# Kernel optimization log

Hardware: AMD Instinct MI355X
Metric: run time of the kernel (lower is better)

## Reference

```python
import jax, jax.numpy as jnp
import numpy as np

B, C, L = 2048, 9605, 8
ALPHA = 0.5        # self.alpha
ALPHA1 = 0.05      # margin
ALPHA2 = 2.0       # asymmetric scale when violated
ALPHA3 = 5.0       # logistic sharpness
ALPHA_OTHER = 0.3  # floor on top-k threshold
TOPK = 16          # x_sorted[15] -> 16th largest


def setup_inputs() -> dict:
    key = jax.random.key(0)
    k1, k2, k3, k4 = jax.random.split(key, 4)
    x = jax.random.normal(k1, (B, C), dtype=jnp.float32)
    # each class assigned to one of 5*L slots; slots < L are whitelist groups,
    # the rest are 'other' classes (like total_indices in the torch code)
    gid = jax.random.randint(k4, (C,), 0, 5 * L)
    gid = gid.at[:L].set(jnp.arange(L))  # guarantee every group is non-empty
    group_mask = gid[None, :] == jnp.arange(L)[:, None]  # [L, C] bool
    # sparse multi-label binarized targets (~14 positives/sample)
    y = (jax.random.uniform(k2, (B, C)) < 0.0015).astype(jnp.float32)
    y_neg = (jax.random.uniform(k3, (B, C)) < 0.0015).astype(jnp.float32)
    return {"x": x, "y": y, "y_neg": y_neg, "group_mask": group_mask}


def _rank_loss(x1, x2):
    # our_rank_loss: sigmoid(alpha3*(x2-x1+margin)), scaled by alpha2 when violated
    d = x2 - x1 + ALPHA1
    s = jax.nn.sigmoid(ALPHA3 * d)
    return jnp.where(d > 0, ALPHA2 * s, s)


def reference(x, y, y_neg, group_mask):
    xs = jax.nn.sigmoid(x)  # [B, C]
    # top_k_thres = max(16th-largest sigmoid score, alpha_other)
    thres = jnp.maximum(jax.lax.top_k(xs, TOPK)[0][:, TOPK - 1], ALPHA_OTHER)  # [B]
    maskf = group_mask.astype(xs.dtype)  # [L, C]
    neg_inf = jnp.array(-jnp.inf, xs.dtype)
    # per-sample max score inside each whitelist group: [B, L]
    group_max = jnp.max(jnp.where(group_mask[None, :, :], xs[:, None, :], neg_inf), axis=-1)
    # find_gt_whitelist: group is 'hit' if any positive target inside it
    gt = (y @ maskf.T) > 0        # [B, L]
    gt_neg = (y_neg @ maskf.T) > 0  # [B, L]
    has_gt = jnp.any(gt, axis=-1)    # [B]; False <=> sentinel len(all_labels)
    has_neg = jnp.any(gt_neg, axis=-1)
    # ---- case B: sample hits at least one whitelist group ----
    rl_correct = _rank_loss(group_max, thres[:, None])    # gt groups above thres
    rl_incorrect = _rank_loss(thres[:, None], group_max)  # non-gt groups below thres
    caseB = jnp.sum(jnp.where(gt, rl_correct, rl_incorrect), axis=-1)  # [B]
    # ---- case A: no whitelist group hit ----
    union = jnp.any(group_mask, axis=0)  # [C] union of all whitelist classes
    union_max = jnp.max(jnp.where(union[None, :], xs, neg_inf), axis=-1)  # [B]
    neg_max = jnp.max(jnp.where(gt_neg, group_max, neg_inf), axis=-1)
    neg_score = jnp.where(has_neg, neg_max, jnp.zeros((), xs.dtype))  # torch starts at 0
    caseA = (1.0 - ALPHA) * _rank_loss(thres, union_max) + ALPHA * _rank_loss(thres, neg_score)
    loss_rank_all = jnp.where(has_gt, caseB, caseA)  # [B]
    return jnp.mean(loss_rank_all)
```

## Files before the change

### kernel.cpp

```cpp
#include <hip/hip_runtime.h>
#include <math.h>

constexpr int B_ = 2048;
constexpr int C_ = 9605;
constexpr int L_ = 8;
constexpr int TOPK_ = 16;
constexpr int CAPQ_ = 512;
constexpr float T0_ = 2.0f;
constexpr int CPAD_ = 9728;

__device__ __forceinline__ float sigm(float v) { return 1.0f / (1.0f + expf(-v)); }

__device__ __forceinline__ float rank_loss(float x1, float x2) {
  float d = x2 - x1 + 0.05f;
  float s = 1.0f / (1.0f + expf(-5.0f * d));
  return (d > 0.0f) ? 2.0f * s : s;
}

__device__ __forceinline__ unsigned int fkey(float v) {
  unsigned int u = __float_as_uint(v);
  return u ^ ((u & 0x80000000u) ? 0xFFFFFFFFu : 0x80000000u);
}
__device__ __forceinline__ float fkeyinv(unsigned int k) {
  unsigned int u = (k & 0x80000000u) ? (k ^ 0x80000000u) : ~k;
  return __uint_as_float(u);
}

__global__ void build_code_kernel(const int* __restrict__ mask,
                                  unsigned char* __restrict__ code) {
  int c = blockIdx.x * 256 + threadIdx.x;
  if (c >= CPAD_) return;
  unsigned char cd = 0xFF;
  if (c < C_) {
#pragma unroll
    for (int l = L_ - 1; l >= 0; --l)
      if (mask[l * C_ + c] != 0) cd = (unsigned char)l;
  }
  code[c] = cd;
}

__global__ void __launch_bounds__(512, 4) row_loss_kernel(
    const float* __restrict__ x, const float* __restrict__ y,
    const float* __restrict__ yn, const unsigned char* __restrict__ code,
    float* __restrict__ loss) {
  __shared__ unsigned int lds_code[2404];
  __shared__ float4 cand4[CAPQ_];
  __shared__ unsigned int gslot[L_];
  __shared__ int cand_cnt;
  __shared__ unsigned int gt_bits, gtn_bits;
  __shared__ float s_x16;
  __shared__ int s_flag, s_red;

  const int t = threadIdx.x;
  const int b = blockIdx.x;
  const int lead = (4 - ((b * C_) & 3)) & 3;
  const int n4 = (C_ - lead) >> 2;

  const float* xb = x + (size_t)(b * C_ + lead);
  const float* yb = y + (size_t)(b * C_ + lead);
  const float* nb = yn + (size_t)(b * C_ + lead);

  if (t < L_) gslot[t] = 0x80000000u;
  if (t == 0) { cand_cnt = 0; gt_bits = 0u; gtn_bits = 0u; s_flag = 0; }

  const unsigned int* cdw = (const unsigned int*)code;
  if (lead == 0) {
    for (int j = t; j < n4; j += 512) lds_code[j] = cdw[j];
  } else {
    const int sh = lead << 3;
    for (int j = t; j < n4; j += 512) {
      unsigned int d0 = cdw[j], d1 = cdw[j + 1];
      lds_code[j] = (d0 >> sh) | (d1 << (32 - sh));
    }
  }
  __syncthreads();

  float4 XA, YA, NA, XB, YB, NB;

  auto ISSUE = [&](int j, float4& X, float4& Y, float4& N) {
    int js = (j < n4) ? j : 0;
    unsigned int vo = (unsigned int)js << 4;
    asm volatile("global_load_dwordx4 %0, %1, %2" : "=v"(X) : "v"(vo), "s"(xb));
    asm volatile("global_load_dwordx4 %0, %1, %2" : "=v"(Y) : "v"(vo), "s"(yb));
    asm volatile("global_load_dwordx4 %0, %1, %2" : "=v"(N) : "v"(vo), "s"(nb));
  };

  auto PROC = [&](const float4& X, const float4& Y, const float4& N, int j) {
    if (j >= n4) return;
    unsigned int cw = lds_code[j];
    float mx = fmaxf(fmaxf(X.x, X.y), fmaxf(X.z, X.w));
    if (mx > T0_) {
      int p = atomicAdd(&cand_cnt, 1);
      if (p < CAPQ_) cand4[p] = X;
    }
    {
      unsigned int cd, k;
      cd = cw & 0xFFu;
      if (cd < 8u && X.x > 0.0f) { k = __float_as_uint(X.x) | 0x80000000u; if (k > gslot[cd]) atomicMax(&gslot[cd], k); }
      cd = (cw >> 8) & 0xFFu;
      if (cd < 8u && X.y > 0.0f) { k = __float_as_uint(X.y) | 0x80000000u; if (k > gslot[cd]) atomicMax(&gslot[cd], k); }
      cd = (cw >> 16) & 0xFFu;
      if (cd < 8u && X.z > 0.0f) { k = __float_as_uint(X.z) | 0x80000000u; if (k > gslot[cd]) atomicMax(&gslot[cd], k); }
      cd = cw >> 24;
      if (cd < 8u && X.w > 0.0f) { k = __float_as_uint(X.w) | 0x80000000u; if (k > gslot[cd]) atomicMax(&gslot[cd], k); }
    }
    float sy = Y.x + Y.y + Y.z + Y.w + N.x + N.y + N.z + N.w;
    if (sy > 0.0f) {
      unsigned int d;
      d = cw & 0xFFu;
      if (d < 8u) { if (Y.x > 0.0f && !((gt_bits >> d) & 1u)) atomicOr(&gt_bits, 1u << d); if (N.x > 0.0f && !((gtn_bits >> d) & 1u)) atomicOr(&gtn_bits, 1u << d); }
      d = (cw >> 8) & 0xFFu;
      if (d < 8u) { if (Y.y > 0.0f && !((gt_bits >> d) & 1u)) atomicOr(&gt_bits, 1u << d); if (N.y > 0.0f && !((gtn_bits >> d) & 1u)) atomicOr(&gtn_bits, 1u << d); }
      d = (cw >> 16) & 0xFFu;
      if (d < 8u) { if (Y.z > 0.0f && !((gt_bits >> d) & 1u)) atomicOr(&gt_bits, 1u << d); if (N.z > 0.0f && !((gtn_bits >> d) & 1u)) atomicOr(&gtn_bits, 1u << d); }
      d = cw >> 24;
      if (d < 8u) { if (Y.w > 0.0f && !((gt_bits >> d) & 1u)) atomicOr(&gt_bits, 1u << d); if (N.w > 0.0f && !((gtn_bits >> d) & 1u)) atomicOr(&gtn_bits, 1u << d); }
    }
  };

  ISSUE(t, XA, YA, NA);
  ISSUE(t + 512, XB, YB, NB);

  asm volatile("s_waitcnt vmcnt(3)" ::: "memory");
  __builtin_amdgcn_sched_barrier(0);
  PROC(XA, YA, NA, t);
  ISSUE(t + 1024, XA, YA, NA);

  asm volatile("s_waitcnt vmcnt(3)" ::: "memory");
  __builtin_amdgcn_sched_barrier(0);
  PROC(XB, YB, NB, t + 512);
  ISSUE(t + 1536, XB, YB, NB);

  asm volatile("s_waitcnt vmcnt(3)" ::: "memory");
  __builtin_amdgcn_sched_barrier(0);
  PROC(XA, YA, NA, t + 1024);
  ISSUE(t + 2048, XA, YA, NA);

  asm volatile("s_waitcnt vmcnt(3)" ::: "memory");
  __builtin_amdgcn_sched_barrier(0);
  PROC(XB, YB, NB, t + 1536);

  asm volatile("s_waitcnt vmcnt(0)" ::: "memory");
  __builtin_amdgcn_sched_barrier(0);
  PROC(XA, YA, NA, t + 2048);

  if (t < 4) {
    auto sc = [&](int c) {
      float xv = x[(size_t)b * C_ + c], yv = y[(size_t)b * C_ + c],
            nv = yn[(size_t)b * C_ + c];
      unsigned int cd = code[c];
      if (cd < 8u) {
        if (xv > 0.0f) atomicMax(&gslot[cd], __float_as_uint(xv) | 0x80000000u);
        if (yv > 0.0f) atomicOr(&gt_bits, 1u << cd);
        if (nv > 0.0f) atomicOr(&gtn_bits, 1u << cd);
      }
      if (xv > T0_) {
        int p = atomicAdd(&cand_cnt, 1);
        if (p < CAPQ_) cand4[p] = make_float4(xv, -INFINITY, -INFINITY, -INFINITY);
      }
    };
    if (t < lead) sc(t);
    int c2 = lead + (n4 << 2) + t;
    if (c2 < C_) sc(c2);
  }
  __syncthreads();

  const int qn = cand_cnt;
  const bool ok_path = (qn >= 4) && (qn <= CAPQ_);
  if (ok_path && t < 64) {
    const float* cf = reinterpret_cast<const float*>(cand4);
    const int nvv = qn << 2;
    unsigned int ku[32];
#pragma unroll
    for (int k = 0; k < 32; ++k) {
      int i = t + (k << 6);
      ku[k] = (i < nvv) ? fkey(cf[i]) : 0u;
    }
    unsigned int lo = 0u, hi = 0xFFFFFFFFu;
#pragma unroll 1
    for (int it = 0; it < 32 && lo < hi; ++it) {
      unsigned int mid = lo + ((hi - lo) >> 1) + 1u;
      int c16 = 0;
#pragma unroll
      for (int k = 0; k < 32; ++k) c16 += (ku[k] >= mid) ? 1 : 0;
#pragma unroll
      for (int off = 32; off > 0; off >>= 1) c16 += __shfl_xor(c16, off, 64);
      if (c16 >= TOPK_) lo = mid; else hi = mid - 1u;
    }
    if (t == 0) {
      float v = fkeyinv(lo);
      s_x16 = v;
      s_flag = (v > T0_) ? 1 : 0;
    }
  }
  __syncthreads();
  if (!(ok_path && s_flag != 0)) {
    const float* xr = x + (size_t)b * C_;
    unsigned int lo = 0u, hi = 0xFFFFFFFFu;
    for (int it = 0; it < 32; ++it) {
      if (lo >= hi) break;
      unsigned int mid = lo + ((hi - lo) >> 1) + 1u;
      if (t == 0) s_red = 0;
      __syncthreads();
      int cl = 0;
      for (int c = t; c < C_; c += 512) cl += (fkey(xr[c]) >= mid) ? 1 : 0;
      atomicAdd(&s_red, cl);
      __syncthreads();
      int total = s_red;
      __syncthreads();
      if (total >= TOPK_) lo = mid; else hi = mid - 1u;
    }
    if (t == 0) s_x16 = fkeyinv(lo);
  }
  __syncthreads();

  if (t == 0) {
    float thres = fmaxf(sigm(s_x16), 0.3f);
    unsigned int gtb = gt_bits, gnb = gtn_bits;
    float caseB = 0.0f, unio = -INFINITY, negmax = -INFINITY;
#pragma unroll
    for (int l = 0; l < L_; ++l) {
      float gm = __uint_as_float(gslot[l] ^ 0x80000000u);
      float g = sigm(gm);
      unio = fmaxf(unio, g);
      caseB += ((gtb >> l) & 1u) ? rank_loss(g, thres) : rank_loss(thres, g);
      if ((gnb >> l) & 1u) negmax = fmaxf(negmax, g);
    }
    float negscore = (gnb != 0u) ? negmax : 0.0f;
    float caseA = 0.5f * rank_loss(thres, unio) + 0.5f * rank_loss(thres, negscore);
    loss[b] = (gtb != 0u) ? caseB : caseA;
  }
}

__global__ void mean_kernel(const float* __restrict__ loss, float* __restrict__ out) {
  const int t = threadIdx.x;
  float s = 0.0f;
  for (int i = t; i < B_; i += 256) s += loss[i];
#pragma unroll
  for (int off = 32; off > 0; off >>= 1) s += __shfl_xor(s, off, 64);
  __shared__ float part[4];
  if ((t & 63) == 0) part[t >> 6] = s;
  __syncthreads();
  if (t == 0) out[0] = (part[0] + part[1] + part[2] + part[3]) * (1.0f / (float)B_);
}

extern "C" void kernel_launch(void* const* d_in, const int* in_sizes, int n_in,
                              void* d_out, int out_size, void* d_ws, size_t ws_size,
                              hipStream_t stream) {
  const float* x = (const float*)d_in[0];
  const float* y = (const float*)d_in[1];
  const float* yn = (const float*)d_in[2];
  const int* mask = (const int*)d_in[3];

  float* loss = (float*)d_ws;
  unsigned char* code = (unsigned char*)d_ws + B_ * sizeof(float);

  hipLaunchKernelGGL(build_code_kernel, dim3((CPAD_ + 255) / 256), dim3(256), 0,
                     stream, mask, code);
  hipLaunchKernelGGL(row_loss_kernel, dim3(B_), dim3(512), 0, stream,
                     x, y, yn, code, loss);
  hipLaunchKernelGGL(mean_kernel, dim3(1), dim3(256), 0, stream,
                     loss, (float*)d_out);
}
```

Baseline: 257.1 us.

## Replace per-row kernel with flat grid-stride sweep plus candidate-based top-k finish

Replaces the one-block-per-row loss kernel with a flat sweep over all B*C elements using float4 loads. The sweep accumulates per-row group maxima and target bits through shared and global atomics, and collects logits above a fixed threshold as top-k candidates. A separate finish kernel binary-searches the 16th largest value among the candidates, falls back to a full row scan when a row has too few or too many candidates, then computes the per-row loss. The goal is better memory-level parallelism and less per-row reduction work. The cost is extra atomics, a setup/zeroing kernel, and a larger workspace; when the workspace is too small the old path still runs.

```diff
diff --git a/kernel.cpp b/kernel.cpp
--- a/kernel.cpp
+++ b/kernel.cpp
@@ -6,8 +6,11 @@
 constexpr int L_ = 8;
 constexpr int TOPK_ = 16;
 constexpr int CAPQ_ = 512;
+constexpr int CAPC_ = 512;
 constexpr float T0_ = 2.0f;
 constexpr int CPAD_ = 9728;
+constexpr int CS_ = 9632;
+constexpr int CHCAP_ = 64;
 
 __device__ __forceinline__ float sigm(float v) { return 1.0f / (1.0f + expf(-v)); }
 
@@ -25,6 +28,193 @@
   unsigned int u = (k & 0x80000000u) ? (k ^ 0x80000000u) : ~k;
   return __uint_as_float(u);
 }
+
+
+__global__ void setup_kernel(const int* __restrict__ mask,
+                             unsigned char* __restrict__ code4,
+                             unsigned int* __restrict__ gslotG,
+                             unsigned int* __restrict__ gtG,
+                             unsigned int* __restrict__ gtnG,
+                             int* __restrict__ cntG) {
+  const int tid = blockIdx.x * 256 + threadIdx.x;
+  if (tid < CS_ + 3) {
+    unsigned char cd = 0xFF;
+    if (tid < C_) {
+#pragma unroll
+      for (int l = L_ - 1; l >= 0; --l)
+        if (mask[l * C_ + tid] != 0) cd = (unsigned char)l;
+    }
+#pragma unroll
+    for (int ld = 0; ld < 4; ++ld) {
+      int p = tid - ld;
+      if (p >= 0 && p < CS_) code4[ld * CS_ + p] = cd;
+    }
+  }
+  for (int i = tid; i < B_ * 8; i += 9728) gslotG[i] = 0x80000000u;
+  for (int i = tid; i < B_; i += 9728) { gtG[i] = 0u; gtnG[i] = 0u; cntG[i] = 0; }
+}
+
+__global__ void __launch_bounds__(256, 8) sweep_kernel(
+    const float* __restrict__ x, const float* __restrict__ y,
+    const float* __restrict__ yn, const unsigned char* __restrict__ code4,
+    unsigned int* __restrict__ gslotG, unsigned int* __restrict__ gtG,
+    unsigned int* __restrict__ gtnG, int* __restrict__ cntG,
+    float* __restrict__ candG) {
+  constexpr int NE = B_ * C_;
+  constexpr int TT = 2048 * 256;
+  constexpr int NSTEP = (NE / 4 + TT - 1) / TT;
+  __shared__ unsigned int ls[16];
+  __shared__ unsigned int lbits[2];
+  __shared__ float lcand[2][CHCAP_];
+  __shared__ int lcnt[2], lbase[2];
+  const int t = threadIdx.x;
+
+  for (int step = 0; step < NSTEP; ++step) {
+    const int qbase = step * TT + (int)blockIdx.x * 256;
+    const int e0 = (qbase + t) << 2;
+    const int efirst = qbase << 2;
+    const int rfirst = efirst / C_;
+    const bool act = (e0 < NE);
+    float4 X, Y, N;
+    if (act) {
+      X = *reinterpret_cast<const float4*>(x + e0);
+      Y = *reinterpret_cast<const float4*>(y + e0);
+      N = *reinterpret_cast<const float4*>(yn + e0);
+    }
+    if (t < 16) ls[t] = 0x80000000u;
+    if (t < 2) { lbits[t] = 0u; lcnt[t] = 0; }
+    __syncthreads();
+
+    if (act) {
+      int r0 = e0 / C_;
+      int cc = e0 - r0 * C_;
+      int rr = r0 - rfirst;
+      const bool fast = (cc + 3 < C_);
+      unsigned int cw = 0u;
+      if (fast)
+        cw = *reinterpret_cast<const unsigned int*>(
+            code4 + (size_t)((cc & 3) * CS_ + (cc & ~3)));
+      const float xv[4] = {X.x, X.y, X.z, X.w};
+      const float yv[4] = {Y.x, Y.y, Y.z, Y.w};
+      const float nv[4] = {N.x, N.y, N.z, N.w};
+#pragma unroll
+      for (int k = 0; k < 4; ++k) {
+        unsigned int cd = fast ? ((cw >> (8 * k)) & 0xFFu)
+                               : (unsigned int)code4[cc];
+        float xk = xv[k];
+        if (cd < 8u) {
+          if (xk > 0.0f) {
+            unsigned int key = __float_as_uint(xk) | 0x80000000u;
+            int a = rr * 8 + (int)cd;
+            if (key > ls[a]) atomicMax(&ls[a], key);
+          }
+          if (yv[k] > 0.0f) atomicOr(&lbits[rr], 1u << cd);
+          if (nv[k] > 0.0f) atomicOr(&lbits[rr], 1u << (8 + cd));
+        }
+        if (xk > T0_) {
+          int p = atomicAdd(&lcnt[rr], 1);
+          if (p < CHCAP_) {
+            lcand[rr][p] = xk;
+          } else {
+            int g = atomicAdd(&cntG[rfirst + rr], 1);
+            if (g < CAPC_) candG[(size_t)(rfirst + rr) * CAPC_ + g] = xk;
+          }
+        }
+        if (++cc == C_) { cc = 0; ++rr; }
+      }
+    }
+    __syncthreads();
+
+    if (t < 16) {
+      unsigned int v = ls[t];
+      int row = rfirst + (t >> 3);
+      if (v != 0x80000000u && row < B_) atomicMax(&gslotG[row * 8 + (t & 7)], v);
+    }
+    if (t < 2) {
+      int row = rfirst + t;
+      unsigned int bb = lbits[t];
+      if (row < B_ && bb != 0u) {
+        unsigned int g8 = bb & 0xFFu, n8 = (bb >> 8) & 0xFFu;
+        if (g8) atomicOr(&gtG[row], g8);
+        if (n8) atomicOr(&gtnG[row], n8);
+      }
+      int n = lcnt[t]; if (n > CHCAP_) n = CHCAP_;
+      lbase[t] = (n > 0 && row < B_) ? atomicAdd(&cntG[row], n) : 0;
+    }
+    __syncthreads();
+#pragma unroll
+    for (int li = 0; li < 2; ++li) {
+      int n = lcnt[li]; if (n > CHCAP_) n = CHCAP_;
+      if (t < n) {
+        int pos = lbase[li] + t;
+        if (pos < CAPC_) candG[(size_t)(rfirst + li) * CAPC_ + pos] = lcand[li][t];
+      }
+    }
+    __syncthreads();
+  }
+}
+
+__global__ void finish_kernel(
+    const float* __restrict__ x, const unsigned int* __restrict__ gslotG,
+    const unsigned int* __restrict__ gtG, const unsigned int* __restrict__ gtnG,
+    const int* __restrict__ cntG, const float* __restrict__ candG,
+    float* __restrict__ loss) {
+  const int r = blockIdx.x;
+  const int t = threadIdx.x;
+  const int cnt = cntG[r];
+  float x16;
+  if (cnt >= TOPK_ && cnt <= CAPC_) {
+    const float* cf = candG + (size_t)r * CAPC_;
+    unsigned int ku[CAPC_ / 64];
+#pragma unroll
+    for (int k = 0; k < CAPC_ / 64; ++k) {
+      int i = t + (k << 6);
+      ku[k] = (i < cnt) ? fkey(cf[i]) : 0u;
+    }
+    unsigned int lo = 0u, hi = 0xFFFFFFFFu;
+#pragma unroll 1
+    for (int it = 0; it < 32 && lo < hi; ++it) {
+      unsigned int mid = lo + ((hi - lo) >> 1) + 1u;
+      int c16 = 0;
+#pragma unroll
+      for (int k = 0; k < CAPC_ / 64; ++k) c16 += (ku[k] >= mid) ? 1 : 0;
+#pragma unroll
+      for (int off = 32; off > 0; off >>= 1) c16 += __shfl_xor(c16, off, 64);
+      if (c16 >= TOPK_) lo = mid; else hi = mid - 1u;
+    }
+    x16 = fkeyinv(lo);
+  } else {
+    const float* xr = x + (size_t)r * C_;
+    unsigned int lo = 0u, hi = 0xFFFFFFFFu;
+#pragma unroll 1
+    for (int it = 0; it < 32 && lo < hi; ++it) {
+      unsigned int mid = lo + ((hi - lo) >> 1) + 1u;
+      int cl = 0;
+      for (int c = t; c < C_; c += 64) cl += (fkey(xr[c]) >= mid) ? 1 : 0;
+#pragma unroll
+      for (int off = 32; off > 0; off >>= 1) cl += __shfl_xor(cl, off, 64);
+      if (cl >= TOPK_) lo = mid; else hi = mid - 1u;
+    }
+    x16 = fkeyinv(lo);
+  }
+  if (t == 0) {
+    float thres = fmaxf(sigm(x16), 0.3f);
+    unsigned int gtb = gtG[r], gnb = gtnG[r];
+    float caseB = 0.0f, unio = -INFINITY, negmax = -INFINITY;
+#pragma unroll
+    for (int l = 0; l < L_; ++l) {
+      float gm = __uint_as_float(gslotG[r * 8 + l] ^ 0x80000000u);
+      float g = sigm(gm);
+      unio = fmaxf(unio, g);
+      caseB += ((gtb >> l) & 1u) ? rank_loss(g, thres) : rank_loss(thres, g);
+      if ((gnb >> l) & 1u) negmax = fmaxf(negmax, g);
+    }
+    float negscore = (gnb != 0u) ? negmax : 0.0f;
+    float caseA = 0.5f * rank_loss(thres, unio) + 0.5f * rank_loss(thres, negscore);
+    loss[r] = (gtb != 0u) ? caseB : caseA;
+  }
+}
+
 
 __global__ void build_code_kernel(const int* __restrict__ mask,
                                   unsigned char* __restrict__ code) {
@@ -252,13 +442,38 @@
   const float* yn = (const float*)d_in[2];
   const int* mask = (const int*)d_in[3];
 
-  float* loss = (float*)d_ws;
-  unsigned char* code = (unsigned char*)d_ws + B_ * sizeof(float);
-
-  hipLaunchKernelGGL(build_code_kernel, dim3((CPAD_ + 255) / 256), dim3(256), 0,
-                     stream, mask, code);
-  hipLaunchKernelGGL(row_loss_kernel, dim3(B_), dim3(512), 0, stream,
-                     x, y, yn, code, loss);
+  constexpr size_t OFF_LOSS = 0;
+  constexpr size_t OFF_CODE4 = 8192;
+  constexpr size_t OFF_GSLOT = OFF_CODE4 + 4 * CS_;
+  constexpr size_t OFF_GT = OFF_GSLOT + B_ * 8 * 4;
+  constexpr size_t OFF_GTN = OFF_GT + B_ * 4;
+  constexpr size_t OFF_CNT = OFF_GTN + B_ * 4;
+  constexpr size_t OFF_CAND = OFF_CNT + B_ * 4;
+  constexpr size_t WS_BIG = OFF_CAND + (size_t)B_ * CAPC_ * 4;
+
+  float* loss = (float*)((char*)d_ws + OFF_LOSS);
+
+  if (ws_size >= WS_BIG) {
+    unsigned char* code4 = (unsigned char*)d_ws + OFF_CODE4;
+    unsigned int* gslotG = (unsigned int*)((char*)d_ws + OFF_GSLOT);
+    unsigned int* gtG = (unsigned int*)((char*)d_ws + OFF_GT);
+    unsigned int* gtnG = (unsigned int*)((char*)d_ws + OFF_GTN);
+    int* cntG = (int*)((char*)d_ws + OFF_CNT);
+    float* candG = (float*)((char*)d_ws + OFF_CAND);
+
+    hipLaunchKernelGGL(setup_kernel, dim3(38), dim3(256), 0, stream,
+                       mask, code4, gslotG, gtG, gtnG, cntG);
+    hipLaunchKernelGGL(sweep_kernel, dim3(2048), dim3(256), 0, stream,
+                       x, y, yn, code4, gslotG, gtG, gtnG, cntG, candG);
+    hipLaunchKernelGGL(finish_kernel, dim3(2048), dim3(64), 0, stream,
+                       x, gslotG, gtG, gtnG, cntG, candG, loss);
+  } else {
+    unsigned char* code = (unsigned char*)d_ws + B_ * sizeof(float);
+    hipLaunchKernelGGL(build_code_kernel, dim3((CPAD_ + 255) / 256), dim3(256), 0,
+                       stream, mask, code);
+    hipLaunchKernelGGL(row_loss_kernel, dim3(B_), dim3(512), 0, stream,
+                       x, y, yn, code, loss);
+  }
   hipLaunchKernelGGL(mean_kernel, dim3(1), dim3(256), 0, stream,
                      loss, (float*)d_out);
 }
```

Result: no change. 256.0 us (-0.4%).
